# Kernel tuning notes

Measured on AMD Instinct MI355X. Metric: run time of the kernel, lower is better.

The kernel has to match this reference:

```python
import jax, jax.numpy as jnp
import numpy as np

N, F_IN, H, C, D, NH, L, FF = 4096, 256, 2, 64, 128, 4, 2, 2048
DEG = 32


def setup_inputs() -> dict:
    key = jax.random.key(0)
    ks = jax.random.split(key, 32)
    s = 0.05
    # graph: random edges + self loops (PyG GATConv adds self loops)
    src = jax.random.randint(ks[0], (N * DEG,), 0, N)
    dst = jax.random.randint(ks[1], (N * DEG,), 0, N)
    loop = jnp.arange(N)
    edge_index = jnp.stack([jnp.concatenate([src, loop]),
                            jnp.concatenate([dst, loop])]).astype(jnp.int64)
    inp = {
        'x': jax.random.normal(ks[2], (N, F_IN), jnp.float32),
        'edge_index': edge_index,
        'enc_w1': jax.random.normal(ks[3], (F_IN, 128), jnp.float32) * s,
        'enc_b1': jnp.zeros((128,), jnp.float32),
        'enc_w2': jax.random.normal(ks[4], (128, D), jnp.float32) * s,
        'enc_b2': jnp.zeros((D,), jnp.float32),
        'gat_w': jax.random.normal(ks[5], (D, H * C), jnp.float32) * s,
        'gat_asrc': jax.random.normal(ks[6], (H, C), jnp.float32) * s,
        'gat_adst': jax.random.normal(ks[7], (H, C), jnp.float32) * s,
        'gat_bias': jnp.zeros((H * C,), jnp.float32),
        't_wq': jax.random.normal(ks[8], (L, D, D), jnp.float32) * s,
        't_bq': jnp.zeros((L, D), jnp.float32),
        't_wk': jax.random.normal(ks[9], (L, D, D), jnp.float32) * s,
        't_bk': jnp.zeros((L, D), jnp.float32),
        't_wv': jax.random.normal(ks[10], (L, D, D), jnp.float32) * s,
        't_bv': jnp.zeros((L, D), jnp.float32),
        't_wo': jax.random.normal(ks[11], (L, D, D), jnp.float32) * s,
        't_bo': jnp.zeros((L, D), jnp.float32),
        't_ln1_g': jnp.ones((L, D), jnp.float32),
        't_ln1_b': jnp.zeros((L, D), jnp.float32),
        't_ln2_g': jnp.ones((L, D), jnp.float32),
        't_ln2_b': jnp.zeros((L, D), jnp.float32),
        't_w1': jax.random.normal(ks[12], (L, D, FF), jnp.float32) * s,
        't_b1': jnp.zeros((L, FF), jnp.float32),
        't_w2': jax.random.normal(ks[13], (L, FF, D), jnp.float32) * s,
        't_b2': jnp.zeros((L, D), jnp.float32),
    }
    return inp


def _layer_norm(v, g, b):
    m = v.mean(-1, keepdims=True)
    var = v.var(-1, keepdims=True)
    return (v - m) / jnp.sqrt(var + 1e-5) * g + b


def _forward(x, edge_index, enc_w1, enc_b1, enc_w2, enc_b2,
             gat_w, gat_asrc, gat_adst, gat_bias,
             t_wq, t_bq, t_wk, t_bk, t_wv, t_bv, t_wo, t_bo,
             t_ln1_g, t_ln1_b, t_ln2_g, t_ln2_b, t_w1, t_b1, t_w2, t_b2):
    n = x.shape[0]
    # encoder MLP: Linear -> ReLU -> Linear
    h = jnp.maximum(x @ enc_w1 + enc_b1, 0.0) @ enc_w2 + enc_b2  # [N, D]
    # GATConv (concat heads), dropout inactive (eval)
    heads, ch = gat_asrc.shape
    hh = (h @ gat_w).reshape(n, heads, ch)                       # [N, H, C]
    src, dst = edge_index[0], edge_index[1]
    a_src = (hh * gat_asrc).sum(-1)                              # [N, H]
    a_dst = (hh * gat_adst).sum(-1)
    e = jax.nn.leaky_relu(a_src[src] + a_dst[dst], 0.2)          # [E, H]
    # segment softmax over destination nodes
    e_max = jax.ops.segment_max(e, dst, num_segments=n)
    e_exp = jnp.exp(e - e_max[dst])
    denom = jax.ops.segment_sum(e_exp, dst, num_segments=n)
    alpha = e_exp / denom[dst]                                   # [E, H]
    agg = jax.ops.segment_sum(alpha[:, :, None] * hh[src], dst, num_segments=n)
    y = agg.reshape(n, heads * ch) + gat_bias                    # [N, D]
    # TransformerEncoder (post-LN, relu FFN), unbatched sequence of N nodes
    d = y.shape[-1]
    dh = d // NH
    for l in range(t_wq.shape[0]):
        q = (y @ t_wq[l] + t_bq[l]).reshape(n, NH, dh)
        k = (y @ t_wk[l] + t_bk[l]).reshape(n, NH, dh)
        v = (y @ t_wv[l] + t_bv[l]).reshape(n, NH, dh)
        scores = jnp.einsum('nhd,mhd->hnm', q, k) / jnp.sqrt(jnp.float32(dh))
        p = jax.nn.softmax(scores, axis=-1)
        a = jnp.einsum('hnm,mhd->nhd', p, v).reshape(n, d)
        a = a @ t_wo[l] + t_bo[l]
        y = _layer_norm(y + a, t_ln1_g[l], t_ln1_b[l])
        f = jnp.maximum(y @ t_w1[l] + t_b1[l], 0.0) @ t_w2[l] + t_b2[l]
        y = _layer_norm(y + f, t_ln2_g[l], t_ln2_b[l])
    return y


def reference(x, edge_index, enc_w1, enc_b1, enc_w2, enc_b2,
              gat_w, gat_asrc, gat_adst, gat_bias,
              t_wq, t_bq, t_wk, t_bk, t_wv, t_bv, t_wo, t_bo,
              t_ln1_g, t_ln1_b, t_ln2_g, t_ln2_b, t_w1, t_b1, t_w2, t_b2):
    return _forward(x, edge_index, enc_w1, enc_b1, enc_w2, enc_b2,
                    gat_w, gat_asrc, gat_adst, gat_bias,
                    t_wq, t_bq, t_wk, t_bk, t_wv, t_bv, t_wo, t_bo,
                    t_ln1_g, t_ln1_b, t_ln2_g, t_ln2_b, t_w1, t_b1, t_w2, t_b2)
```

## Files before the change

kernel.cpp:

```cpp
#include <hip/hip_runtime.h>

typedef unsigned short u16;
typedef unsigned int u32;
typedef __attribute__((ext_vector_type(8))) short bh8;
typedef __attribute__((ext_vector_type(4))) float fx4;
typedef __attribute__((ext_vector_type(4))) short s4;
typedef __attribute__((ext_vector_type(2))) unsigned int u32x2;

#define QS 0.2550437194342803f

__device__ __forceinline__ u16 f2bf(float f) {
    unsigned u = __float_as_uint(f);
    u += 0x7fffu + ((u >> 16) & 1u);
    return (u16)(u >> 16);
}

__device__ __forceinline__ u32 cvtpk(float lo, float hi) {
    u32 r;
    asm("v_cvt_pk_bf16_f32 %0, %1, %2" : "=v"(r) : "v"(lo), "v"(hi));
    return r;
}

__global__ __launch_bounds__(256) void prep_kernel(
    const float* x, const float* ew1, const float* ew2, const float* gw,
    const float* wq, const float* wk, const float* wv, const float* wo,
    const float* w1, const float* w2,
    const float* bq, const float* bk, const float* bv,
    u16* xb, u16* ew1t, u16* ew2t, u16* gwt,
    u16* wqkvt, float* bqkv, u16* wot, u16* w1t, u16* w2t)
{
    __shared__ u16 tile[64 * 65];
    int bid = blockIdx.x;
    const int t = threadIdx.x;

    if (bid < 128) {
        const float4* x4 = (const float4*)x;
        s4* o4 = (s4*)xb;
        #pragma unroll
        for (int i = 0; i < 8; i++) {
            int fi = bid * 2048 + i * 256 + t;
            float4 v = x4[fi];
            s4 o = { (short)f2bf(v.x), (short)f2bf(v.y), (short)f2bf(v.z), (short)f2bf(v.w) };
            o4[fi] = o;
        }
        return;
    }
    bid -= 128;
    if (bid < 1) {
        for (int idx = t; idx < 768; idx += 256) {
            int l = idx / 384, n = idx % 384;
            float v;
            if (n < 128)      v = bq[l * 128 + n] * QS;
            else if (n < 256) v = bk[l * 128 + n - 128];
            else              v = bv[l * 128 + n - 256];
            bqkv[idx] = v;
        }
        return;
    }
    bid -= 1;

    const float* src; u16* dst; int R, C, tr, tc; float sc = 1.f;
    if (bid < 8)            { src = ew1; dst = ew1t; R = 256; C = 128; tr = bid >> 1; tc = bid & 1; }
    else if ((bid -= 8) < 4)  { src = ew2; dst = ew2t; R = 128; C = 128; tr = bid >> 1; tc = bid & 1; }
    else if ((bid -= 4) < 4)  { src = gw;  dst = gwt;  R = 128; C = 128; tr = bid >> 1; tc = bid & 1; }
    else if ((bid -= 4) < 24) {
        int l = bid / 12, r2 = bid % 12, which = r2 >> 2, i = r2 & 3;
        R = 128; C = 128; tr = i >> 1; tc = i & 1;
        if (which == 0)      { src = wq + l * 16384; dst = wqkvt + l * 49152;         sc = QS; }
        else if (which == 1) { src = wk + l * 16384; dst = wqkvt + l * 49152 + 16384; }
        else                 { src = wv + l * 16384; dst = wqkvt + l * 49152 + 32768; }
    }
    else if ((bid -= 24) < 8)   { int l = bid >> 2, i = bid & 3;  src = wo + l * 16384; dst = wot + l * 16384; R = 128; C = 128; tr = i >> 1; tc = i & 1; }
    else if ((bid -= 8) < 128)  { int l = bid >> 6, i = bid & 63; src = w1 + (size_t)l * 262144; dst = w1t + (size_t)l * 262144; R = 128;  C = 2048; tr = i & 1;  tc = i >> 1; }
    else { bid -= 128;            int l = bid >> 6, i = bid & 63; src = w2 + (size_t)l * 262144; dst = w2t + (size_t)l * 262144; R = 2048; C = 128;  tr = i >> 1; tc = i & 1; }

    const int r = t >> 2, cs = (t & 3) * 16;
    const float* sp = src + (size_t)(tr * 64 + r) * C + tc * 64 + cs;
    #pragma unroll
    for (int j = 0; j < 16; j++) tile[r * 65 + cs + j] = f2bf(sp[j] * sc);
    __syncthreads();
    u16* dp = dst + (size_t)(tc * 64 + r) * R + tr * 64 + cs;
    #pragma unroll
    for (int j = 0; j < 16; j++) dp[j] = tile[(cs + j) * 65 + r];
}

__global__ __launch_bounds__(256) void gemm_bf16(
    const u16* __restrict__ A, const u16* __restrict__ Bt,
    const float* __restrict__ bias,
    float* __restrict__ Cf, u16* __restrict__ Cb, float* __restrict__ Cpart,
    u16* __restrict__ Cvt,
    int M, int N, int K, int relu, int kchunk, int ldc)
{
    __shared__ __align__(16) u16 As[2][64][40];
    __shared__ __align__(16) u16 Bs[2][64][40];
    const int m0 = blockIdx.x * 64, n0 = blockIdx.y * 64, z = blockIdx.z;
    const int tid = threadIdx.x;
    const int lane = tid & 63, w = tid >> 6;
    const int wm = (w >> 1) * 32, wn = (w & 1) * 32;
    const int l15 = lane & 15, l4 = lane >> 4;
    const int srow = tid >> 2, skq = (tid & 3) * 8;
    const int k0 = z * kchunk;

    const u16* Ap = A + (size_t)(m0 + srow) * K + k0 + skq;
    const u16* Bp = Bt + (size_t)(n0 + srow) * K + k0 + skq;

    fx4 acc00 = {0,0,0,0}, acc01 = {0,0,0,0}, acc10 = {0,0,0,0}, acc11 = {0,0,0,0};

    *(int4*)&As[0][srow][skq] = *(const int4*)Ap;
    *(int4*)&Bs[0][srow][skq] = *(const int4*)Bp;

    const int niter = kchunk >> 5;
    for (int it = 0; it < niter; it++) {
        const int cur = it & 1;
        int4 ar, br;
        __syncthreads();
        if (it + 1 < niter) {
            ar = *(const int4*)(Ap + (it + 1) * 32);
            br = *(const int4*)(Bp + (it + 1) * 32);
        }
        bh8 a0 = *(const bh8*)&As[cur][wm + l15][l4 * 8];
        bh8 a1 = *(const bh8*)&As[cur][wm + 16 + l15][l4 * 8];
        bh8 b0 = *(const bh8*)&Bs[cur][wn + l15][l4 * 8];
        bh8 b1 = *(const bh8*)&Bs[cur][wn + 16 + l15][l4 * 8];
        acc00 = __builtin_amdgcn_mfma_f32_16x16x32_bf16(a0, b0, acc00, 0, 0, 0);
        acc01 = __builtin_amdgcn_mfma_f32_16x16x32_bf16(a0, b1, acc01, 0, 0, 0);
        acc10 = __builtin_amdgcn_mfma_f32_16x16x32_bf16(a1, b0, acc10, 0, 0, 0);
        acc11 = __builtin_amdgcn_mfma_f32_16x16x32_bf16(a1, b1, acc11, 0, 0, 0);
        if (it + 1 < niter) {
            *(int4*)&As[cur ^ 1][srow][skq] = ar;
            *(int4*)&Bs[cur ^ 1][srow][skq] = br;
        }
    }

    fx4* accs[2][2] = {{&acc00, &acc01}, {&acc10, &acc11}};
    #pragma unroll
    for (int i = 0; i < 2; i++)
        #pragma unroll
        for (int j = 0; j < 2; j++) {
            int colg = n0 + wn + j * 16 + l15;
            int rowb = m0 + wm + i * 16 + l4 * 4;
            if (Cpart) {
                float* cp = Cpart + (size_t)z * M * N;
                #pragma unroll
                for (int r = 0; r < 4; r++)
                    cp[(size_t)(rowb + r) * N + colg] = (*accs[i][j])[r];
                continue;
            }
            float bvv = bias ? bias[colg] : 0.f;
            float vals[4];
            #pragma unroll
            for (int r = 0; r < 4; r++) {
                float v = (*accs[i][j])[r] + bvv;
                vals[r] = relu ? fmaxf(v, 0.f) : v;
            }
            if (Cvt && colg >= 256) {
                s4 pk = { (short)f2bf(vals[0]), (short)f2bf(vals[1]),
                          (short)f2bf(vals[2]), (short)f2bf(vals[3]) };
                *(s4*)&Cvt[(size_t)(colg - 256) * 4096 + rowb] = pk;
            } else {
                #pragma unroll
                for (int r = 0; r < 4; r++) {
                    if (Cf) Cf[(size_t)(rowb + r) * ldc + colg] = vals[r];
                    if (Cb) Cb[(size_t)(rowb + r) * ldc + colg] = f2bf(vals[r]);
                }
            }
        }
}

__global__ __launch_bounds__(128) void gat_prep(
    const float* __restrict__ hh, const float* __restrict__ asrc,
    const float* __restrict__ adst, float* __restrict__ an_src,
    float* __restrict__ an_dst)
{
    int n = blockIdx.x, tid = threadIdx.x;
    int head = tid >> 6, c = tid & 63;
    float v = hh[n * 128 + tid];
    float ps = v * asrc[head * 64 + c];
    float pd = v * adst[head * 64 + c];
    for (int off = 32; off; off >>= 1) { ps += __shfl_down(ps, off); pd += __shfl_down(pd, off); }
    if (c == 0) { an_src[n * 2 + head] = ps; an_dst[n * 2 + head] = pd; }
}

__global__ void count_edges(const int* __restrict__ dst, int* counts, int E) {
    int i = blockIdx.x * 256 + threadIdx.x;
    if (i < E) atomicAdd(&counts[dst[i]], 1);
}

__global__ __launch_bounds__(1024) void scan_kernel(const int* __restrict__ counts,
                                                    int* row_start, int* cursor) {
    __shared__ int s[1024];
    int tid = threadIdx.x, b = tid * 4;
    int c0 = counts[b], c1 = counts[b+1], c2 = counts[b+2], c3 = counts[b+3];
    int sum = c0 + c1 + c2 + c3;
    s[tid] = sum;
    __syncthreads();
    for (int off = 1; off < 1024; off <<= 1) {
        int v = (tid >= off) ? s[tid - off] : 0;
        __syncthreads();
        s[tid] += v;
        __syncthreads();
    }
    int excl = s[tid] - sum;
    int r0 = excl, r1 = excl + c0, r2 = r1 + c1, r3 = r2 + c2;
    row_start[b] = r0; row_start[b+1] = r1; row_start[b+2] = r2; row_start[b+3] = r3;
    cursor[b] = r0; cursor[b+1] = r1; cursor[b+2] = r2; cursor[b+3] = r3;
    if (tid == 1023) row_start[4096] = s[1023];
}

__global__ void scatter_edges(const int* __restrict__ src, const int* __restrict__ dst,
                              int* cursor, int* csr_src, int E) {
    int i = blockIdx.x * 256 + threadIdx.x;
    if (i < E) { int pos = atomicAdd(&cursor[dst[i]], 1); csr_src[pos] = src[i]; }
}

__global__ __launch_bounds__(256) void gat_aggregate(
    const int* __restrict__ row_start, const int* __restrict__ csr_src,
    const float* __restrict__ an_src, const float* __restrict__ an_dst,
    const float* __restrict__ hh, const float* __restrict__ gbias,
    float* __restrict__ y32, u16* __restrict__ yb)
{
    int n = blockIdx.x, tid = threadIdx.x;
    const int lane = tid & 63, wv = tid >> 6;
    int start = row_start[n], end = row_start[n + 1];
    float ad0 = an_dst[n * 2 + 0], ad1 = an_dst[n * 2 + 1];
    __shared__ float rmx[4][2], rsm[4][2];
    __shared__ float sal0[128], sal1[128], sagg[256];
    __shared__ int sidx[128];

    float mx0 = -1e30f, mx1 = -1e30f;
    for (int i = start + tid; i < end; i += 256) {
        int s = csr_src[i];
        float e0 = an_src[s * 2 + 0] + ad0; e0 = e0 > 0.f ? e0 : 0.2f * e0;
        float e1 = an_src[s * 2 + 1] + ad1; e1 = e1 > 0.f ? e1 : 0.2f * e1;
        mx0 = fmaxf(mx0, e0); mx1 = fmaxf(mx1, e1);
    }
    for (int off = 32; off; off >>= 1) { mx0 = fmaxf(mx0, __shfl_down(mx0, off)); mx1 = fmaxf(mx1, __shfl_down(mx1, off)); }
    if (lane == 0) { rmx[wv][0] = mx0; rmx[wv][1] = mx1; }
    __syncthreads();
    mx0 = fmaxf(fmaxf(rmx[0][0], rmx[1][0]), fmaxf(rmx[2][0], rmx[3][0]));
    mx1 = fmaxf(fmaxf(rmx[0][1], rmx[1][1]), fmaxf(rmx[2][1], rmx[3][1]));

    float den0 = 0.f, den1 = 0.f;
    for (int i = start + tid; i < end; i += 256) {
        int s = csr_src[i];
        float e0 = an_src[s * 2 + 0] + ad0; e0 = e0 > 0.f ? e0 : 0.2f * e0;
        float e1 = an_src[s * 2 + 1] + ad1; e1 = e1 > 0.f ? e1 : 0.2f * e1;
        den0 += __expf(e0 - mx0); den1 += __expf(e1 - mx1);
    }
    for (int off = 32; off; off >>= 1) { den0 += __shfl_down(den0, off); den1 += __shfl_down(den1, off); }
    if (lane == 0) { rsm[wv][0] = den0; rsm[wv][1] = den1; }
    __syncthreads();
    den0 = rsm[0][0] + rsm[1][0] + rsm[2][0] + rsm[3][0];
    den1 = rsm[0][1] + rsm[1][1] + rsm[2][1] + rsm[3][1];
    float rd0 = 1.f / den0, rd1 = 1.f / den1;

    const int grp = tid >> 7, ch = tid & 127, head = ch >> 6;
    float agg = 0.f;
    for (int c0 = start; c0 < end; c0 += 128) {
        int cnt = min(128, end - c0);
        __syncthreads();
        if (tid < cnt) {
            int s = csr_src[c0 + tid];
            float e0 = an_src[s * 2 + 0] + ad0; e0 = e0 > 0.f ? e0 : 0.2f * e0;
            float e1 = an_src[s * 2 + 1] + ad1; e1 = e1 > 0.f ? e1 : 0.2f * e1;
            sal0[tid] = __expf(e0 - mx0) * rd0;
            sal1[tid] = __expf(e1 - mx1) * rd1;
            sidx[tid] = s;
        }
        __syncthreads();
        const float* sal = head ? sal1 : sal0;
        for (int j = grp; j < cnt; j += 2)
            agg += sal[j] * hh[(size_t)sidx[j] * 128 + ch];
    }
    sagg[tid] = agg;
    __syncthreads();
    if (tid < 128) {
        float v = sagg[tid] + sagg[tid + 128] + gbias[tid];
        y32[(size_t)n * 128 + tid] = v;
        yb[(size_t)n * 128 + tid] = f2bf(v);
    }
}

__global__ __launch_bounds__(256) void flash_attn_part(
    const u16* __restrict__ q, const u16* __restrict__ k,
    const u16* __restrict__ vt, float* __restrict__ po,
    float* __restrict__ pm, float* __restrict__ pl)
{
    __shared__ __align__(16) u16 Kb[2][64][40];
    __shared__ __align__(16) u16 Vb[2][32][72];
    __shared__ __align__(16) u16 Ps[4][16][72];
    const int q0 = blockIdx.x * 64, h = blockIdx.y, ch = blockIdx.z;
    const int tid = threadIdx.x;
    const int w = tid >> 6, lane = tid & 63, l15 = lane & 15, l4 = lane >> 4;

    bh8 qf = *(const bh8*)&q[(size_t)(q0 + w * 16 + l15) * 256 + h * 32 + l4 * 8];

    const int skey = tid >> 2, sds = (tid & 3) * 8;
    const int svd = tid >> 3, svk = (tid & 7) * 8;
    const u16* kgp = &k[(size_t)(ch * 512 + skey) * 256 + h * 32 + sds];
    const u16* vgp = &vt[(size_t)(h * 32 + svd) * 4096 + ch * 512 + svk];

    fx4 o0 = {0,0,0,0}, o1 = {0,0,0,0};
    float M = -1e30f, L = 0.f;

    *(int4*)&Kb[0][skey][sds] = *(const int4*)kgp;
    *(int4*)&Vb[0][svd][svk] = *(const int4*)vgp;

    for (int ti = 0; ti < 8; ti++) {
        const int cur = ti & 1;
        int4 kr, vr;
        __syncthreads();
        if (ti < 7) {
            kr = *(const int4*)(kgp + (size_t)(ti + 1) * 64 * 256);
            vr = *(const int4*)(vgp + (ti + 1) * 64);
        }

        fx4 s[4];
        #pragma unroll
        for (int sub = 0; sub < 4; sub++) {
            bh8 kf = *(const bh8*)&Kb[cur][sub * 16 + l15][l4 * 8];
            fx4 z = {0,0,0,0};
            s[sub] = __builtin_amdgcn_mfma_f32_16x16x32_bf16(kf, qf, z, 0, 0, 0);
        }
        float t0 = fmaxf(fmaxf(s[0][0], s[0][1]), s[0][2]);
        float t1 = fmaxf(fmaxf(s[0][3], s[1][0]), s[1][1]);
        float t2 = fmaxf(fmaxf(s[1][2], s[1][3]), s[2][0]);
        float t3 = fmaxf(fmaxf(s[2][1], s[2][2]), s[2][3]);
        float t4 = fmaxf(fmaxf(s[3][0], s[3][1]), s[3][2]);
        float pmax = fmaxf(fmaxf(fmaxf(t0, t1), t2), fmaxf(fmaxf(t3, t4), s[3][3]));
        pmax = fmaxf(pmax, __shfl_xor(pmax, 16));
        pmax = fmaxf(pmax, __shfl_xor(pmax, 32));
        if (!__all(pmax - M <= 8.0f)) {
            float f = __builtin_amdgcn_exp2f(M - pmax);
            M = pmax;
            o0 *= f; o1 *= f; L *= f;
        }

        #pragma unroll
        for (int sub = 0; sub < 4; sub++)
            #pragma unroll
            for (int r = 0; r < 4; r++)
                s[sub][r] = __builtin_amdgcn_exp2f(s[sub][r] - M);
        float ss0 = (s[0][0] + s[0][1]) + (s[0][2] + s[0][3]);
        float ss1 = (s[1][0] + s[1][1]) + (s[1][2] + s[1][3]);
        float ss2 = (s[2][0] + s[2][1]) + (s[2][2] + s[2][3]);
        float ss3 = (s[3][0] + s[3][1]) + (s[3][2] + s[3][3]);
        float lsum = (ss0 + ss1) + (ss2 + ss3);
        lsum += __shfl_xor(lsum, 16);
        lsum += __shfl_xor(lsum, 32);
        L += lsum;

        #pragma unroll
        for (int sub = 0; sub < 4; sub++) {
            u32x2 pk = { cvtpk(s[sub][0], s[sub][1]), cvtpk(s[sub][2], s[sub][3]) };
            *(u32x2*)&Ps[w][l15][sub * 16 + l4 * 4] = pk;
        }

        #pragma unroll
        for (int kc = 0; kc < 2; kc++) {
            bh8 bf  = *(const bh8*)&Ps[w][l15][kc * 32 + l4 * 8];
            bh8 af0 = *(const bh8*)&Vb[cur][l15][kc * 32 + l4 * 8];
            bh8 af1 = *(const bh8*)&Vb[cur][16 + l15][kc * 32 + l4 * 8];
            o0 = __builtin_amdgcn_mfma_f32_16x16x32_bf16(af0, bf, o0, 0, 0, 0);
            o1 = __builtin_amdgcn_mfma_f32_16x16x32_bf16(af1, bf, o1, 0, 0, 0);
        }

        if (ti < 7) {
            *(int4*)&Kb[cur ^ 1][skey][sds] = kr;
            *(int4*)&Vb[cur ^ 1][svd][svk] = vr;
        }
    }
    const int base = (blockIdx.x * 4 + h) * 8 + ch;
    const int qrow = w * 16 + l15;
    *(fx4*)&po[(size_t)(base * 64 + qrow) * 32 + l4 * 4]      = o0;
    *(fx4*)&po[(size_t)(base * 64 + qrow) * 32 + 16 + l4 * 4] = o1;
    if (l4 == 0) { pm[base * 64 + qrow] = M; pl[base * 64 + qrow] = L; }
}

__global__ __launch_bounds__(256) void attn_combine(
    const float* __restrict__ po, const float* __restrict__ pm,
    const float* __restrict__ pl, u16* __restrict__ out)
{
    int qb = blockIdx.x, h = blockIdx.y;
    int col = threadIdx.x & 31, r0 = threadIdx.x >> 5;
    int rb = (qb * 4 + h) * 8;
    for (int j = 0; j < 8; j++) {
        int row = r0 * 8 + j;
        float m = -1e30f;
        for (int c = 0; c < 8; c++) m = fmaxf(m, pm[(rb + c) * 64 + row]);
        float l = 0.f, o = 0.f;
        for (int c = 0; c < 8; c++) {
            float wgt = __builtin_amdgcn_exp2f(pm[(rb + c) * 64 + row] - m);
            l += wgt * pl[(rb + c) * 64 + row];
            o += wgt * po[(size_t)((rb + c) * 64 + row) * 32 + col];
        }
        out[(size_t)(qb * 64 + row) * 128 + h * 32 + col] = f2bf(o / l);
    }
}

__global__ __launch_bounds__(128) void add_ln(
    const float* __restrict__ y, const float* __restrict__ delta,
    const float* __restrict__ g, const float* __restrict__ b,
    float* __restrict__ out32, u16* __restrict__ outb)
{
    int n = blockIdx.x, tid = threadIdx.x;
    float v = y[(size_t)n * 128 + tid] + delta[(size_t)n * 128 + tid];
    float sacc = v;
    for (int off = 32; off; off >>= 1) sacc += __shfl_down(sacc, off);
    __shared__ float sm[2], sv[2];
    if ((tid & 63) == 0) sm[tid >> 6] = sacc;
    __syncthreads();
    float mean = (sm[0] + sm[1]) * (1.f / 128.f);
    float d = v - mean;
    float qacc = d * d;
    for (int off = 32; off; off >>= 1) qacc += __shfl_down(qacc, off);
    if ((tid & 63) == 0) sv[tid >> 6] = qacc;
    __syncthreads();
    float var = (sv[0] + sv[1]) * (1.f / 128.f);
    float o = d * rsqrtf(var + 1e-5f) * g[tid] + b[tid];
    out32[(size_t)n * 128 + tid] = o;
    outb[(size_t)n * 128 + tid] = f2bf(o);
}

__global__ __launch_bounds__(128) void add_ln8(
    const float* __restrict__ y, const float* __restrict__ part,
    const float* __restrict__ bias,
    const float* __restrict__ g, const float* __restrict__ b,
    float* __restrict__ out32, u16* __restrict__ outb)
{
    int n = blockIdx.x, tid = threadIdx.x;
    float v = y[(size_t)n * 128 + tid] + bias[tid];
    for (int z = 0; z < 8; z++) v += part[(size_t)z * 524288 + n * 128 + tid];
    float sacc = v;
    for (int off = 32; off; off >>= 1) sacc += __shfl_down(sacc, off);
    __shared__ float sm[2], sv[2];
    if ((tid & 63) == 0) sm[tid >> 6] = sacc;
    __syncthreads();
    float mean = (sm[0] + sm[1]) * (1.f / 128.f);
    float d = v - mean;
    float qacc = d * d;
    for (int off = 32; off; off >>= 1) qacc += __shfl_down(qacc, off);
    if ((tid & 63) == 0) sv[tid >> 6] = qacc;
    __syncthreads();
    float var = (sv[0] + sv[1]) * (1.f / 128.f);
    float o = d * rsqrtf(var + 1e-5f) * g[tid] + b[tid];
    out32[(size_t)n * 128 + tid] = o;
    outb[(size_t)n * 128 + tid] = f2bf(o);
}

extern "C" void kernel_launch(void* const* d_in, const int* in_sizes, int n_in,
                              void* d_out, int out_size, void* d_ws, size_t ws_size,
                              hipStream_t stream)
{
    const float* x     = (const float*)d_in[0];
    const int*   ei    = (const int*)  d_in[1];
    const float* ew1   = (const float*)d_in[2];
    const float* eb1   = (const float*)d_in[3];
    const float* ew2   = (const float*)d_in[4];
    const float* eb2   = (const float*)d_in[5];
    const float* gw    = (const float*)d_in[6];
    const float* gasrc = (const float*)d_in[7];
    const float* gadst = (const float*)d_in[8];
    const float* gbias = (const float*)d_in[9];
    const float* wq    = (const float*)d_in[10];
    const float* bq    = (const float*)d_in[11];
    const float* wk    = (const float*)d_in[12];
    const float* bk    = (const float*)d_in[13];
    const float* wv    = (const float*)d_in[14];
    const float* bv    = (const float*)d_in[15];
    const float* wo    = (const float*)d_in[16];
    const float* bo    = (const float*)d_in[17];
    const float* ln1g  = (const float*)d_in[18];
    const float* ln1b  = (const float*)d_in[19];
    const float* ln2g  = (const float*)d_in[20];
    const float* ln2b  = (const float*)d_in[21];
    const float* w1    = (const float*)d_in[22];
    const float* b1    = (const float*)d_in[23];
    const float* w2    = (const float*)d_in[24];
    const float* b2    = (const float*)d_in[25];

    const int E = in_sizes[1] / 2;
    const int* esrc = ei;
    const int* edst = ei + E;

    char* p = (char*)d_ws;
    auto alloc = [&](size_t bytes) -> void* {
        void* r = (void*)p;
        p += (bytes + 255) & ~(size_t)255;
        return r;
    };
    u16* xb    = (u16*)alloc(4096 * 256 * 2);
    u16* ew1t  = (u16*)alloc(128 * 256 * 2);
    u16* ew2t  = (u16*)alloc(128 * 128 * 2);
    u16* gwt   = (u16*)alloc(128 * 128 * 2);
    u16* wqkvt = (u16*)alloc(2 * 384 * 128 * 2);
    float* bqkv = (float*)alloc(2 * 384 * 4);
    u16* wot   = (u16*)alloc(2 * 128 * 128 * 2);
    u16* w1t   = (u16*)alloc(2 * 2048 * 128 * 2);
    u16* w2t   = (u16*)alloc(2 * 128 * 2048 * 2);
    u16* h1b   = (u16*)alloc(4096 * 128 * 2);
    u16* hb    = (u16*)alloc(4096 * 128 * 2);
    float* hh  = (float*)alloc(4096 * 128 * 4);
    float* ansrc = (float*)alloc(4096 * 2 * 4);
    float* andst = (float*)alloc(4096 * 2 * 4);
    int* counts    = (int*)alloc(4096 * 4);
    int* row_start = (int*)alloc(4097 * 4);
    int* cursor    = (int*)alloc(4096 * 4);
    int* csr_src   = (int*)alloc((size_t)E * 4);
    float* y32 = (float*)alloc(4096 * 128 * 4);
    u16* yb    = (u16*)alloc(4096 * 128 * 2);
    u16* qkvb  = (u16*)alloc((size_t)4096 * 256 * 2);
    u16* vtb   = (u16*)alloc(4096 * 128 * 2);
    u16* attnb = (u16*)alloc(4096 * 128 * 2);
    float* po  = (float*)alloc((size_t)64 * 4 * 8 * 64 * 32 * 4);
    float* pm  = (float*)alloc(64 * 4 * 8 * 64 * 4);
    float* pl  = (float*)alloc(64 * 4 * 8 * 64 * 4);
    float* proj32 = (float*)alloc(4096 * 128 * 4);
    u16* ff1b  = (u16*)alloc((size_t)4096 * 2048 * 2);
    float* ff2part = (float*)alloc((size_t)8 * 4096 * 128 * 4);

    prep_kernel<<<433, 256, 0, stream>>>(x, ew1, ew2, gw, wq, wk, wv, wo, w1, w2,
                                         bq, bk, bv,
                                         xb, ew1t, ew2t, gwt, wqkvt, bqkv, wot, w1t, w2t);

    gemm_bf16<<<dim3(64, 2), 256, 0, stream>>>(xb, ew1t, eb1, nullptr, h1b, nullptr, nullptr, 4096, 128, 256, 1, 256, 128);
    gemm_bf16<<<dim3(64, 2), 256, 0, stream>>>(h1b, ew2t, eb2, nullptr, hb, nullptr, nullptr, 4096, 128, 128, 0, 128, 128);

    gemm_bf16<<<dim3(64, 2), 256, 0, stream>>>(hb, gwt, nullptr, hh, nullptr, nullptr, nullptr, 4096, 128, 128, 0, 128, 128);
    gat_prep<<<4096, 128, 0, stream>>>(hh, gasrc, gadst, ansrc, andst);
    hipMemsetAsync(counts, 0, 4096 * sizeof(int), stream);
    count_edges<<<(E + 255) / 256, 256, 0, stream>>>(edst, counts, E);
    scan_kernel<<<1, 1024, 0, stream>>>(counts, row_start, cursor);
    scatter_edges<<<(E + 255) / 256, 256, 0, stream>>>(esrc, edst, cursor, csr_src, E);
    gat_aggregate<<<4096, 256, 0, stream>>>(row_start, csr_src, ansrc, andst, hh, gbias, y32, yb);

    for (int l = 0; l < 2; l++) {
        gemm_bf16<<<dim3(64, 6), 256, 0, stream>>>(yb, wqkvt + l * 49152, bqkv + l * 384, nullptr, qkvb, nullptr, vtb, 4096, 384, 128, 0, 128, 256);
        flash_attn_part<<<dim3(64, 4, 8), 256, 0, stream>>>(qkvb, qkvb + 128, vtb, po, pm, pl);
        attn_combine<<<dim3(64, 4), 256, 0, stream>>>(po, pm, pl, attnb);
        gemm_bf16<<<dim3(64, 2), 256, 0, stream>>>(attnb, wot + l * 16384, bo + l * 128, proj32, nullptr, nullptr, nullptr, 4096, 128, 128, 0, 128, 128);
        add_ln<<<4096, 128, 0, stream>>>(y32, proj32, ln1g + l * 128, ln1b + l * 128, y32, yb);
        gemm_bf16<<<dim3(64, 32), 256, 0, stream>>>(yb, w1t + (size_t)l * 262144, b1 + l * 2048, nullptr, ff1b, nullptr, nullptr, 4096, 2048, 128, 1, 128, 2048);
        gemm_bf16<<<dim3(64, 2, 8), 256, 0, stream>>>(ff1b, w2t + (size_t)l * 262144, nullptr, nullptr, nullptr, ff2part, nullptr, 4096, 128, 2048, 0, 256, 128);
        float* outp = (l == 1) ? (float*)d_out : y32;
        add_ln8<<<4096, 128, 0, stream>>>(y32, ff2part, b2 + l * 128, ln2g + l * 128, ln2b + l * 128, outp, yb);
    }
}
```

Baseline: 209.8 us.

## Template GEMM tile sizes, split-K out-proj, warp-shuffle scan, MFMA priority hints

The GEMM becomes a template over block tile sizes, and the QKV, FF1 and FF2 GEMMs switch to 64x128 tiles so each loaded A tile is reused across more columns. The output projection now uses a 2-way split-K with partial sums reduced inside a generalized add+layernorm kernel. The single-block scan replaces its shared-memory Hillis-Steele loop with wave shuffles, and the flash-attention MFMA sections get s_setprio hints. The larger tiles launch fewer blocks, which may lower occupancy, and the split-K adds partial-buffer traffic.

```diff
diff --git a/kernel.cpp b/kernel.cpp
--- a/kernel.cpp
+++ b/kernel.cpp
@@ -84,73 +84,85 @@
     for (int j = 0; j < 16; j++) dp[j] = tile[(cs + j) * 65 + r];
 }
 
-__global__ __launch_bounds__(256) void gemm_bf16(
+template<int BM, int BN>
+__global__ __launch_bounds__(256) void gemm_t(
     const u16* __restrict__ A, const u16* __restrict__ Bt,
     const float* __restrict__ bias,
     float* __restrict__ Cf, u16* __restrict__ Cb, float* __restrict__ Cpart,
     u16* __restrict__ Cvt,
     int M, int N, int K, int relu, int kchunk, int ldc)
 {
-    __shared__ __align__(16) u16 As[2][64][40];
-    __shared__ __align__(16) u16 Bs[2][64][40];
-    const int m0 = blockIdx.x * 64, n0 = blockIdx.y * 64, z = blockIdx.z;
+    constexpr int NM = BM / 32, NN = BN / 32;
+    constexpr int AI = BM * 4 / 256, BI = BN * 4 / 256;
+    __shared__ __align__(16) u16 As[2][BM][40];
+    __shared__ __align__(16) u16 Bs[2][BN][40];
+    const int m0 = blockIdx.x * BM, n0 = blockIdx.y * BN, z = blockIdx.z;
     const int tid = threadIdx.x;
     const int lane = tid & 63, w = tid >> 6;
-    const int wm = (w >> 1) * 32, wn = (w & 1) * 32;
+    const int wm = (w >> 1) * (BM / 2), wn = (w & 1) * (BN / 2);
     const int l15 = lane & 15, l4 = lane >> 4;
-    const int srow = tid >> 2, skq = (tid & 3) * 8;
     const int k0 = z * kchunk;
 
-    const u16* Ap = A + (size_t)(m0 + srow) * K + k0 + skq;
-    const u16* Bp = Bt + (size_t)(n0 + srow) * K + k0 + skq;
-
-    fx4 acc00 = {0,0,0,0}, acc01 = {0,0,0,0}, acc10 = {0,0,0,0}, acc11 = {0,0,0,0};
-
-    *(int4*)&As[0][srow][skq] = *(const int4*)Ap;
-    *(int4*)&Bs[0][srow][skq] = *(const int4*)Bp;
+    fx4 acc[NM][NN] = {};
+
+    const u16* Apb[AI]; const u16* Bpb[BI];
+    #pragma unroll
+    for (int i = 0; i < AI; i++) { int s = tid + i * 256; Apb[i] = A + (size_t)(m0 + (s >> 2)) * K + k0 + (s & 3) * 8; }
+    #pragma unroll
+    for (int i = 0; i < BI; i++) { int s = tid + i * 256; Bpb[i] = Bt + (size_t)(n0 + (s >> 2)) * K + k0 + (s & 3) * 8; }
+
+    #pragma unroll
+    for (int i = 0; i < AI; i++) { int s = tid + i * 256; *(int4*)&As[0][s >> 2][(s & 3) * 8] = *(const int4*)Apb[i]; }
+    #pragma unroll
+    for (int i = 0; i < BI; i++) { int s = tid + i * 256; *(int4*)&Bs[0][s >> 2][(s & 3) * 8] = *(const int4*)Bpb[i]; }
 
     const int niter = kchunk >> 5;
     for (int it = 0; it < niter; it++) {
         const int cur = it & 1;
-        int4 ar, br;
+        int4 ar[AI], br[BI];
         __syncthreads();
         if (it + 1 < niter) {
-            ar = *(const int4*)(Ap + (it + 1) * 32);
-            br = *(const int4*)(Bp + (it + 1) * 32);
-        }
-        bh8 a0 = *(const bh8*)&As[cur][wm + l15][l4 * 8];
-        bh8 a1 = *(const bh8*)&As[cur][wm + 16 + l15][l4 * 8];
-        bh8 b0 = *(const bh8*)&Bs[cur][wn + l15][l4 * 8];
-        bh8 b1 = *(const bh8*)&Bs[cur][wn + 16 + l15][l4 * 8];
-        acc00 = __builtin_amdgcn_mfma_f32_16x16x32_bf16(a0, b0, acc00, 0, 0, 0);
-        acc01 = __builtin_amdgcn_mfma_f32_16x16x32_bf16(a0, b1, acc01, 0, 0, 0);
-        acc10 = __builtin_amdgcn_mfma_f32_16x16x32_bf16(a1, b0, acc10, 0, 0, 0);
-        acc11 = __builtin_amdgcn_mfma_f32_16x16x32_bf16(a1, b1, acc11, 0, 0, 0);
+            #pragma unroll
+            for (int i = 0; i < AI; i++) ar[i] = *(const int4*)(Apb[i] + (it + 1) * 32);
+            #pragma unroll
+            for (int i = 0; i < BI; i++) br[i] = *(const int4*)(Bpb[i] + (it + 1) * 32);
+        }
+        bh8 af[NM], bf[NN];
+        #pragma unroll
+        for (int mi = 0; mi < NM; mi++) af[mi] = *(const bh8*)&As[cur][wm + mi * 16 + l15][l4 * 8];
+        #pragma unroll
+        for (int nj = 0; nj < NN; nj++) bf[nj] = *(const bh8*)&Bs[cur][wn + nj * 16 + l15][l4 * 8];
+        #pragma unroll
+        for (int mi = 0; mi < NM; mi++)
+            #pragma unroll
+            for (int nj = 0; nj < NN; nj++)
+                acc[mi][nj] = __builtin_amdgcn_mfma_f32_16x16x32_bf16(af[mi], bf[nj], acc[mi][nj], 0, 0, 0);
         if (it + 1 < niter) {
-            *(int4*)&As[cur ^ 1][srow][skq] = ar;
-            *(int4*)&Bs[cur ^ 1][srow][skq] = br;
-        }
-    }
-
-    fx4* accs[2][2] = {{&acc00, &acc01}, {&acc10, &acc11}};
-    #pragma unroll
-    for (int i = 0; i < 2; i++)
-        #pragma unroll
-        for (int j = 0; j < 2; j++) {
-            int colg = n0 + wn + j * 16 + l15;
-            int rowb = m0 + wm + i * 16 + l4 * 4;
+            #pragma unroll
+            for (int i = 0; i < AI; i++) { int s = tid + i * 256; *(int4*)&As[cur ^ 1][s >> 2][(s & 3) * 8] = ar[i]; }
+            #pragma unroll
+            for (int i = 0; i < BI; i++) { int s = tid + i * 256; *(int4*)&Bs[cur ^ 1][s >> 2][(s & 3) * 8] = br[i]; }
+        }
+    }
+
+    #pragma unroll
+    for (int mi = 0; mi < NM; mi++)
+        #pragma unroll
+        for (int nj = 0; nj < NN; nj++) {
+            int colg = n0 + wn + nj * 16 + l15;
+            int rowb = m0 + wm + mi * 16 + l4 * 4;
             if (Cpart) {
                 float* cp = Cpart + (size_t)z * M * N;
                 #pragma unroll
                 for (int r = 0; r < 4; r++)
-                    cp[(size_t)(rowb + r) * N + colg] = (*accs[i][j])[r];
+                    cp[(size_t)(rowb + r) * N + colg] = acc[mi][nj][r];
                 continue;
             }
             float bvv = bias ? bias[colg] : 0.f;
             float vals[4];
             #pragma unroll
             for (int r = 0; r < 4; r++) {
-                float v = (*accs[i][j])[r] + bvv;
+                float v = acc[mi][nj][r] + bvv;
                 vals[r] = relu ? fmaxf(v, 0.f) : v;
             }
             if (Cvt && colg >= 256) {
@@ -188,23 +200,30 @@
 
 __global__ __launch_bounds__(1024) void scan_kernel(const int* __restrict__ counts,
                                                     int* row_start, int* cursor) {
-    __shared__ int s[1024];
-    int tid = threadIdx.x, b = tid * 4;
+    __shared__ int wsum[16];
+    int tid = threadIdx.x, lane = tid & 63, wv = tid >> 6;
+    int b = tid * 4;
     int c0 = counts[b], c1 = counts[b+1], c2 = counts[b+2], c3 = counts[b+3];
     int sum = c0 + c1 + c2 + c3;
-    s[tid] = sum;
-    __syncthreads();
-    for (int off = 1; off < 1024; off <<= 1) {
-        int v = (tid >= off) ? s[tid - off] : 0;
-        __syncthreads();
-        s[tid] += v;
-        __syncthreads();
-    }
-    int excl = s[tid] - sum;
+    int inc = sum;
+    #pragma unroll
+    for (int off = 1; off < 64; off <<= 1) {
+        int v = __shfl_up(inc, off);
+        if (lane >= off) inc += v;
+    }
+    if (lane == 63) wsum[wv] = inc;
+    __syncthreads();
+    int base = 0;
+    #pragma unroll
+    for (int i = 0; i < 16; i++) {
+        int v = wsum[i];
+        base += (i < wv) ? v : 0;
+    }
+    int excl = base + inc - sum;
     int r0 = excl, r1 = excl + c0, r2 = r1 + c1, r3 = r2 + c2;
     row_start[b] = r0; row_start[b+1] = r1; row_start[b+2] = r2; row_start[b+3] = r3;
     cursor[b] = r0; cursor[b+1] = r1; cursor[b+2] = r2; cursor[b+3] = r3;
-    if (tid == 1023) row_start[4096] = s[1023];
+    if (tid == 1023) row_start[4096] = base + inc;
 }
 
 __global__ void scatter_edges(const int* __restrict__ src, const int* __restrict__ dst,
@@ -316,12 +335,14 @@
         }
 
         fx4 s[4];
+        __builtin_amdgcn_s_setprio(1);
         #pragma unroll
         for (int sub = 0; sub < 4; sub++) {
             bh8 kf = *(const bh8*)&Kb[cur][sub * 16 + l15][l4 * 8];
             fx4 z = {0,0,0,0};
             s[sub] = __builtin_amdgcn_mfma_f32_16x16x32_bf16(kf, qf, z, 0, 0, 0);
         }
+        __builtin_amdgcn_s_setprio(0);
         float t0 = fmaxf(fmaxf(s[0][0], s[0][1]), s[0][2]);
         float t1 = fmaxf(fmaxf(s[0][3], s[1][0]), s[1][1]);
         float t2 = fmaxf(fmaxf(s[1][2], s[1][3]), s[2][0]);
@@ -356,6 +377,7 @@
             *(u32x2*)&Ps[w][l15][sub * 16 + l4 * 4] = pk;
         }
 
+        __builtin_amdgcn_s_setprio(1);
         #pragma unroll
         for (int kc = 0; kc < 2; kc++) {
             bh8 bf  = *(const bh8*)&Ps[w][l15][kc * 32 + l4 * 8];
@@ -364,6 +386,7 @@
             o0 = __builtin_amdgcn_mfma_f32_16x16x32_bf16(af0, bf, o0, 0, 0, 0);
             o1 = __builtin_amdgcn_mfma_f32_16x16x32_bf16(af1, bf, o1, 0, 0, 0);
         }
+        __builtin_amdgcn_s_setprio(0);
 
         if (ti < 7) {
             *(int4*)&Kb[cur ^ 1][skey][sds] = kr;
@@ -398,39 +421,15 @@
     }
 }
 
-__global__ __launch_bounds__(128) void add_ln(
-    const float* __restrict__ y, const float* __restrict__ delta,
-    const float* __restrict__ g, const float* __restrict__ b,
-    float* __restrict__ out32, u16* __restrict__ outb)
-{
-    int n = blockIdx.x, tid = threadIdx.x;
-    float v = y[(size_t)n * 128 + tid] + delta[(size_t)n * 128 + tid];
-    float sacc = v;
-    for (int off = 32; off; off >>= 1) sacc += __shfl_down(sacc, off);
-    __shared__ float sm[2], sv[2];
-    if ((tid & 63) == 0) sm[tid >> 6] = sacc;
-    __syncthreads();
-    float mean = (sm[0] + sm[1]) * (1.f / 128.f);
-    float d = v - mean;
-    float qacc = d * d;
-    for (int off = 32; off; off >>= 1) qacc += __shfl_down(qacc, off);
-    if ((tid & 63) == 0) sv[tid >> 6] = qacc;
-    __syncthreads();
-    float var = (sv[0] + sv[1]) * (1.f / 128.f);
-    float o = d * rsqrtf(var + 1e-5f) * g[tid] + b[tid];
-    out32[(size_t)n * 128 + tid] = o;
-    outb[(size_t)n * 128 + tid] = f2bf(o);
-}
-
-__global__ __launch_bounds__(128) void add_ln8(
-    const float* __restrict__ y, const float* __restrict__ part,
+__global__ __launch_bounds__(128) void add_ln_p(
+    const float* __restrict__ y, const float* __restrict__ part, int nz,
     const float* __restrict__ bias,
     const float* __restrict__ g, const float* __restrict__ b,
     float* __restrict__ out32, u16* __restrict__ outb)
 {
     int n = blockIdx.x, tid = threadIdx.x;
     float v = y[(size_t)n * 128 + tid] + bias[tid];
-    for (int z = 0; z < 8; z++) v += part[(size_t)z * 524288 + n * 128 + tid];
+    for (int z = 0; z < nz; z++) v += part[(size_t)z * 524288 + n * 128 + tid];
     float sacc = v;
     for (int off = 32; off; off >>= 1) sacc += __shfl_down(sacc, off);
     __shared__ float sm[2], sv[2];
@@ -515,7 +514,7 @@
     float* po  = (float*)alloc((size_t)64 * 4 * 8 * 64 * 32 * 4);
     float* pm  = (float*)alloc(64 * 4 * 8 * 64 * 4);
     float* pl  = (float*)alloc(64 * 4 * 8 * 64 * 4);
-    float* proj32 = (float*)alloc(4096 * 128 * 4);
+    float* projpart = (float*)alloc((size_t)2 * 4096 * 128 * 4);
     u16* ff1b  = (u16*)alloc((size_t)4096 * 2048 * 2);
     float* ff2part = (float*)alloc((size_t)8 * 4096 * 128 * 4);
 
@@ -523,10 +522,10 @@
                                          bq, bk, bv,
                                          xb, ew1t, ew2t, gwt, wqkvt, bqkv, wot, w1t, w2t);
 
-    gemm_bf16<<<dim3(64, 2), 256, 0, stream>>>(xb, ew1t, eb1, nullptr, h1b, nullptr, nullptr, 4096, 128, 256, 1, 256, 128);
-    gemm_bf16<<<dim3(64, 2), 256, 0, stream>>>(h1b, ew2t, eb2, nullptr, hb, nullptr, nullptr, 4096, 128, 128, 0, 128, 128);
-
-    gemm_bf16<<<dim3(64, 2), 256, 0, stream>>>(hb, gwt, nullptr, hh, nullptr, nullptr, nullptr, 4096, 128, 128, 0, 128, 128);
+    gemm_t<64, 64><<<dim3(64, 2), 256, 0, stream>>>(xb, ew1t, eb1, nullptr, h1b, nullptr, nullptr, 4096, 128, 256, 1, 256, 128);
+    gemm_t<64, 64><<<dim3(64, 2), 256, 0, stream>>>(h1b, ew2t, eb2, nullptr, hb, nullptr, nullptr, 4096, 128, 128, 0, 128, 128);
+
+    gemm_t<64, 64><<<dim3(64, 2), 256, 0, stream>>>(hb, gwt, nullptr, hh, nullptr, nullptr, nullptr, 4096, 128, 128, 0, 128, 128);
     gat_prep<<<4096, 128, 0, stream>>>(hh, gasrc, gadst, ansrc, andst);
     hipMemsetAsync(counts, 0, 4096 * sizeof(int), stream);
     count_edges<<<(E + 255) / 256, 256, 0, stream>>>(edst, counts, E);
@@ -535,14 +534,14 @@
     gat_aggregate<<<4096, 256, 0, stream>>>(row_start, csr_src, ansrc, andst, hh, gbias, y32, yb);
 
     for (int l = 0; l < 2; l++) {
-        gemm_bf16<<<dim3(64, 6), 256, 0, stream>>>(yb, wqkvt + l * 49152, bqkv + l * 384, nullptr, qkvb, nullptr, vtb, 4096, 384, 128, 0, 128, 256);
+        gemm_t<64, 128><<<dim3(64, 3), 256, 0, stream>>>(yb, wqkvt + l * 49152, bqkv + l * 384, nullptr, qkvb, nullptr, vtb, 4096, 384, 128, 0, 128, 256);
         flash_attn_part<<<dim3(64, 4, 8), 256, 0, stream>>>(qkvb, qkvb + 128, vtb, po, pm, pl);
         attn_combine<<<dim3(64, 4), 256, 0, stream>>>(po, pm, pl, attnb);
-        gemm_bf16<<<dim3(64, 2), 256, 0, stream>>>(attnb, wot + l * 16384, bo + l * 128, proj32, nullptr, nullptr, nullptr, 4096, 128, 128, 0, 128, 128);
-        add_ln<<<4096, 128, 0, stream>>>(y32, proj32, ln1g + l * 128, ln1b + l * 128, y32, yb);
-        gemm_bf16<<<dim3(64, 32), 256, 0, stream>>>(yb, w1t + (size_t)l * 262144, b1 + l * 2048, nullptr, ff1b, nullptr, nullptr, 4096, 2048, 128, 1, 128, 2048);
-        gemm_bf16<<<dim3(64, 2, 8), 256, 0, stream>>>(ff1b, w2t + (size_t)l * 262144, nullptr, nullptr, nullptr, ff2part, nullptr, 4096, 128, 2048, 0, 256, 128);
+        gemm_t<64, 64><<<dim3(64, 2, 2), 256, 0, stream>>>(attnb, wot + l * 16384, nullptr, nullptr, nullptr, projpart, nullptr, 4096, 128, 128, 0, 64, 128);
+        add_ln_p<<<4096, 128, 0, stream>>>(y32, projpart, 2, bo + l * 128, ln1g + l * 128, ln1b + l * 128, y32, yb);
+        gemm_t<64, 128><<<dim3(64, 16), 256, 0, stream>>>(yb, w1t + (size_t)l * 262144, b1 + l * 2048, nullptr, ff1b, nullptr, nullptr, 4096, 2048, 128, 1, 128, 2048);
+        gemm_t<64, 128><<<dim3(64, 1, 8), 256, 0, stream>>>(ff1b, w2t + (size_t)l * 262144, nullptr, nullptr, nullptr, ff2part, nullptr, 4096, 128, 2048, 0, 256, 128);
         float* outp = (l == 1) ? (float*)d_out : y32;
-        add_ln8<<<4096, 128, 0, stream>>>(y32, ff2part, b2 + l * 128, ln2g + l * 128, ln2b + l * 128, outp, yb);
-    }
-}
+        add_ln_p<<<4096, 128, 0, stream>>>(y32, ff2part, 8, b2 + l * 128, ln2g + l * 128, ln2b + l * 128, outp, yb);
+    }
+}
```

Result: slower. 237.7 us (+13.3%).

## Fuse output projection with layernorm, shrink FF2 split-K, speed scan, drop memset

Applied to the files above, without the earlier changes.

Adds an oproj_ln kernel that computes the attention output projection with MFMA over 32-row tiles and applies the residual add and layernorm in the same kernel. This removes the proj32 round trip and one launch per layer. The FF2 split-K factor drops from 8 to 4, which halves the partial-sum traffic read by the following layernorm but leaves fewer blocks in that GEMM. The scan now uses wave shuffles instead of a barrier-heavy shared-memory loop, and the counts memset is folded into gat_prep. The fused layernorm computes variance as E[x^2]-mean^2, which can lose some precision.

```diff
diff --git a/kernel.cpp b/kernel.cpp
--- a/kernel.cpp
+++ b/kernel.cpp
@@ -170,9 +170,10 @@
 __global__ __launch_bounds__(128) void gat_prep(
     const float* __restrict__ hh, const float* __restrict__ asrc,
     const float* __restrict__ adst, float* __restrict__ an_src,
-    float* __restrict__ an_dst)
+    float* __restrict__ an_dst, int* __restrict__ counts)
 {
     int n = blockIdx.x, tid = threadIdx.x;
+    if (tid == 0) counts[n] = 0;
     int head = tid >> 6, c = tid & 63;
     float v = hh[n * 128 + tid];
     float ps = v * asrc[head * 64 + c];
@@ -188,23 +189,30 @@
 
 __global__ __launch_bounds__(1024) void scan_kernel(const int* __restrict__ counts,
                                                     int* row_start, int* cursor) {
-    __shared__ int s[1024];
-    int tid = threadIdx.x, b = tid * 4;
+    __shared__ int wsum[16];
+    int tid = threadIdx.x, lane = tid & 63, wv = tid >> 6;
+    int b = tid * 4;
     int c0 = counts[b], c1 = counts[b+1], c2 = counts[b+2], c3 = counts[b+3];
     int sum = c0 + c1 + c2 + c3;
-    s[tid] = sum;
-    __syncthreads();
-    for (int off = 1; off < 1024; off <<= 1) {
-        int v = (tid >= off) ? s[tid - off] : 0;
-        __syncthreads();
-        s[tid] += v;
-        __syncthreads();
-    }
-    int excl = s[tid] - sum;
+    int inc = sum;
+    #pragma unroll
+    for (int off = 1; off < 64; off <<= 1) {
+        int v = __shfl_up(inc, off);
+        if (lane >= off) inc += v;
+    }
+    if (lane == 63) wsum[wv] = inc;
+    __syncthreads();
+    int base = 0;
+    #pragma unroll
+    for (int i = 0; i < 16; i++) {
+        int v = wsum[i];
+        base += (i < wv) ? v : 0;
+    }
+    int excl = base + inc - sum;
     int r0 = excl, r1 = excl + c0, r2 = r1 + c1, r3 = r2 + c2;
     row_start[b] = r0; row_start[b+1] = r1; row_start[b+2] = r2; row_start[b+3] = r3;
     cursor[b] = r0; cursor[b+1] = r1; cursor[b+2] = r2; cursor[b+3] = r3;
-    if (tid == 1023) row_start[4096] = s[1023];
+    if (tid == 1023) row_start[4096] = base + inc;
 }
 
 __global__ void scatter_edges(const int* __restrict__ src, const int* __restrict__ dst,
@@ -398,39 +406,93 @@
     }
 }
 
-__global__ __launch_bounds__(128) void add_ln(
-    const float* __restrict__ y, const float* __restrict__ delta,
-    const float* __restrict__ g, const float* __restrict__ b,
-    float* __restrict__ out32, u16* __restrict__ outb)
-{
-    int n = blockIdx.x, tid = threadIdx.x;
-    float v = y[(size_t)n * 128 + tid] + delta[(size_t)n * 128 + tid];
-    float sacc = v;
-    for (int off = 32; off; off >>= 1) sacc += __shfl_down(sacc, off);
-    __shared__ float sm[2], sv[2];
-    if ((tid & 63) == 0) sm[tid >> 6] = sacc;
-    __syncthreads();
-    float mean = (sm[0] + sm[1]) * (1.f / 128.f);
-    float d = v - mean;
-    float qacc = d * d;
-    for (int off = 32; off; off >>= 1) qacc += __shfl_down(qacc, off);
-    if ((tid & 63) == 0) sv[tid >> 6] = qacc;
-    __syncthreads();
-    float var = (sv[0] + sv[1]) * (1.f / 128.f);
-    float o = d * rsqrtf(var + 1e-5f) * g[tid] + b[tid];
-    out32[(size_t)n * 128 + tid] = o;
-    outb[(size_t)n * 128 + tid] = f2bf(o);
-}
-
-__global__ __launch_bounds__(128) void add_ln8(
-    const float* __restrict__ y, const float* __restrict__ part,
+__global__ __launch_bounds__(256) void oproj_ln(
+    const u16* __restrict__ A, const u16* __restrict__ Bt,
+    const float* __restrict__ bias, const float* __restrict__ g,
+    const float* __restrict__ b,
+    float* __restrict__ y32, u16* __restrict__ yb)
+{
+    __shared__ __align__(16) u16 As[2][32][40];
+    __shared__ __align__(16) u16 Bs[2][128][40];
+    __shared__ float Ct[32][132];
+    const int m0 = blockIdx.x * 32;
+    const int tid = threadIdx.x;
+    const int lane = tid & 63, w = tid >> 6;
+    const int wm = (w >> 1) * 16, wn = (w & 1) * 64;
+    const int l15 = lane & 15, l4 = lane >> 4;
+
+    const int arow = tid >> 2, akq = (tid & 3) * 8;
+    const u16* Ap  = A + (size_t)(m0 + arow) * 128 + akq;
+    const u16* Bp0 = Bt + (size_t)arow * 128 + akq;
+    const u16* Bp1 = Bp0 + (size_t)64 * 128;
+
+    fx4 acc[4] = {};
+
+    if (tid < 128) *(int4*)&As[0][arow][akq] = *(const int4*)Ap;
+    *(int4*)&Bs[0][arow][akq]      = *(const int4*)Bp0;
+    *(int4*)&Bs[0][arow + 64][akq] = *(const int4*)Bp1;
+
+    for (int it = 0; it < 4; it++) {
+        const int cur = it & 1;
+        int4 ar, br0, br1;
+        __syncthreads();
+        if (it < 3) {
+            if (tid < 128) ar = *(const int4*)(Ap + (it + 1) * 32);
+            br0 = *(const int4*)(Bp0 + (it + 1) * 32);
+            br1 = *(const int4*)(Bp1 + (it + 1) * 32);
+        }
+        bh8 af = *(const bh8*)&As[cur][wm + l15][l4 * 8];
+        #pragma unroll
+        for (int nj = 0; nj < 4; nj++) {
+            bh8 bf = *(const bh8*)&Bs[cur][wn + nj * 16 + l15][l4 * 8];
+            acc[nj] = __builtin_amdgcn_mfma_f32_16x16x32_bf16(af, bf, acc[nj], 0, 0, 0);
+        }
+        if (it < 3) {
+            if (tid < 128) *(int4*)&As[cur ^ 1][arow][akq] = ar;
+            *(int4*)&Bs[cur ^ 1][arow][akq]      = br0;
+            *(int4*)&Bs[cur ^ 1][arow + 64][akq] = br1;
+        }
+    }
+
+    #pragma unroll
+    for (int nj = 0; nj < 4; nj++) {
+        int cl = wn + nj * 16 + l15;
+        float bvv = bias[cl];
+        #pragma unroll
+        for (int r = 0; r < 4; r++) {
+            int rl = wm + l4 * 4 + r;
+            Ct[rl][cl] = acc[nj][r] + bvv + y32[(size_t)(m0 + rl) * 128 + cl];
+        }
+    }
+    __syncthreads();
+
+    const int row = tid >> 3, c0 = (tid & 7) * 16;
+    float s1 = 0.f, s2 = 0.f;
+    #pragma unroll
+    for (int j = 0; j < 16; j++) { float v = Ct[row][c0 + j]; s1 += v; s2 += v * v; }
+    #pragma unroll
+    for (int off = 1; off < 8; off <<= 1) { s1 += __shfl_xor(s1, off); s2 += __shfl_xor(s2, off); }
+    float mean = s1 * (1.f / 128.f);
+    float var = s2 * (1.f / 128.f) - mean * mean;
+    float rstd = rsqrtf(var + 1e-5f);
+    #pragma unroll
+    for (int j = 0; j < 16; j++) {
+        int col = c0 + j;
+        float o = (Ct[row][col] - mean) * rstd * g[col] + b[col];
+        y32[(size_t)(m0 + row) * 128 + col] = o;
+        yb[(size_t)(m0 + row) * 128 + col] = f2bf(o);
+    }
+}
+
+__global__ __launch_bounds__(128) void add_ln_p(
+    const float* __restrict__ y, const float* __restrict__ part, int nz,
     const float* __restrict__ bias,
     const float* __restrict__ g, const float* __restrict__ b,
     float* __restrict__ out32, u16* __restrict__ outb)
 {
     int n = blockIdx.x, tid = threadIdx.x;
     float v = y[(size_t)n * 128 + tid] + bias[tid];
-    for (int z = 0; z < 8; z++) v += part[(size_t)z * 524288 + n * 128 + tid];
+    for (int z = 0; z < nz; z++) v += part[(size_t)z * 524288 + n * 128 + tid];
     float sacc = v;
     for (int off = 32; off; off >>= 1) sacc += __shfl_down(sacc, off);
     __shared__ float sm[2], sv[2];
@@ -515,9 +577,8 @@
     float* po  = (float*)alloc((size_t)64 * 4 * 8 * 64 * 32 * 4);
     float* pm  = (float*)alloc(64 * 4 * 8 * 64 * 4);
     float* pl  = (float*)alloc(64 * 4 * 8 * 64 * 4);
-    float* proj32 = (float*)alloc(4096 * 128 * 4);
     u16* ff1b  = (u16*)alloc((size_t)4096 * 2048 * 2);
-    float* ff2part = (float*)alloc((size_t)8 * 4096 * 128 * 4);
+    float* ff2part = (float*)alloc((size_t)4 * 4096 * 128 * 4);
 
     prep_kernel<<<433, 256, 0, stream>>>(x, ew1, ew2, gw, wq, wk, wv, wo, w1, w2,
                                          bq, bk, bv,
@@ -527,8 +588,7 @@
     gemm_bf16<<<dim3(64, 2), 256, 0, stream>>>(h1b, ew2t, eb2, nullptr, hb, nullptr, nullptr, 4096, 128, 128, 0, 128, 128);
 
     gemm_bf16<<<dim3(64, 2), 256, 0, stream>>>(hb, gwt, nullptr, hh, nullptr, nullptr, nullptr, 4096, 128, 128, 0, 128, 128);
-    gat_prep<<<4096, 128, 0, stream>>>(hh, gasrc, gadst, ansrc, andst);
-    hipMemsetAsync(counts, 0, 4096 * sizeof(int), stream);
+    gat_prep<<<4096, 128, 0, stream>>>(hh, gasrc, gadst, ansrc, andst, counts);
     count_edges<<<(E + 255) / 256, 256, 0, stream>>>(edst, counts, E);
     scan_kernel<<<1, 1024, 0, stream>>>(counts, row_start, cursor);
     scatter_edges<<<(E + 255) / 256, 256, 0, stream>>>(esrc, edst, cursor, csr_src, E);
@@ -538,11 +598,10 @@
         gemm_bf16<<<dim3(64, 6), 256, 0, stream>>>(yb, wqkvt + l * 49152, bqkv + l * 384, nullptr, qkvb, nullptr, vtb, 4096, 384, 128, 0, 128, 256);
         flash_attn_part<<<dim3(64, 4, 8), 256, 0, stream>>>(qkvb, qkvb + 128, vtb, po, pm, pl);
         attn_combine<<<dim3(64, 4), 256, 0, stream>>>(po, pm, pl, attnb);
-        gemm_bf16<<<dim3(64, 2), 256, 0, stream>>>(attnb, wot + l * 16384, bo + l * 128, proj32, nullptr, nullptr, nullptr, 4096, 128, 128, 0, 128, 128);
-        add_ln<<<4096, 128, 0, stream>>>(y32, proj32, ln1g + l * 128, ln1b + l * 128, y32, yb);
+        oproj_ln<<<128, 256, 0, stream>>>(attnb, wot + l * 16384, bo + l * 128, ln1g + l * 128, ln1b + l * 128, y32, yb);
         gemm_bf16<<<dim3(64, 32), 256, 0, stream>>>(yb, w1t + (size_t)l * 262144, b1 + l * 2048, nullptr, ff1b, nullptr, nullptr, 4096, 2048, 128, 1, 128, 2048);
-        gemm_bf16<<<dim3(64, 2, 8), 256, 0, stream>>>(ff1b, w2t + (size_t)l * 262144, nullptr, nullptr, nullptr, ff2part, nullptr, 4096, 128, 2048, 0, 256, 128);
+        gemm_bf16<<<dim3(64, 2, 4), 256, 0, stream>>>(ff1b, w2t + (size_t)l * 262144, nullptr, nullptr, nullptr, ff2part, nullptr, 4096, 128, 2048, 0, 512, 128);
         float* outp = (l == 1) ? (float*)d_out : y32;
-        add_ln8<<<4096, 128, 0, stream>>>(y32, ff2part, b2 + l * 128, ln2g + l * 128, ln2b + l * 128, outp, yb);
-    }
-}
+        add_ln_p<<<4096, 128, 0, stream>>>(y32, ff2part, 4, b2 + l * 128, ln2g + l * 128, ln2b + l * 128, outp, yb);
+    }
+}
```

Measured after the change: 199.6 us. 1.05x faster.
